# Kernel tuning notes

Hardware: AMD Instinct MI355X
Metric: run time of the kernel (lower is better)

Reference implementation:

```python
import jax, jax.numpy as jnp
import numpy as np

N, D_IN, H, C, K = 16384, 2048, 4096, 256, 256


def setup_inputs() -> dict:
    key = jax.random.key(0)
    ks = jax.random.split(key, 13)

    def lin(kw, kb, fan_in, fan_out):
        # torch Linear default init: U(-1/sqrt(fan_in), 1/sqrt(fan_in)); stored as [in, out]
        bound = 1.0 / np.sqrt(fan_in)
        W = jax.random.uniform(kw, (fan_in, fan_out), jnp.float32, -bound, bound)
        b = jax.random.uniform(kb, (fan_out,), jnp.float32, -bound, bound)
        return W, b

    W_e1, b_e1 = lin(ks[0], ks[1], D_IN, H)
    W_e2, b_e2 = lin(ks[2], ks[3], H, C)
    W_d1, b_d1 = lin(ks[4], ks[5], C, H)
    W_d2, b_d2 = lin(ks[6], ks[7], H, D_IN)
    # codebooks init U(-1/K, 1/K) per the torch code
    cb1 = jax.random.uniform(ks[8], (K, C), jnp.float32, -1.0 / K, 1.0 / K)
    cb2 = jax.random.uniform(ks[9], (K, C), jnp.float32, -1.0 / K, 1.0 / K)
    cb3 = jax.random.uniform(ks[10], (K, C), jnp.float32, -1.0 / K, 1.0 / K)
    x = jax.random.normal(ks[11], (N, D_IN), jnp.float32)
    return {"x": x, "W_e1": W_e1, "b_e1": b_e1, "W_e2": W_e2, "b_e2": b_e2,
            "cb1": cb1, "cb2": cb2, "cb3": cb3,
            "W_d1": W_d1, "b_d1": b_d1, "W_d2": W_d2, "b_d2": b_d2}


def _vq_stage(z, cb):
    # dist[n,k] = sum_c (cb[k,c] - z[n,c])^2 = ||z||^2 - 2 z.cb^T + ||cb||^2
    # (same math as the torch N x K x C broadcast, expressed as a GEMM)
    d = (jnp.sum(z * z, axis=1, keepdims=True)
         - 2.0 * (z @ cb.T)
         + jnp.sum(cb * cb, axis=1))            # [N, K]
    nearest = jnp.argmin(d, axis=1)             # [N]
    zq = cb[nearest]                            # gather [N, C]
    return nearest, zq


def reference(x, W_e1, b_e1, W_e2, b_e2, cb1, cb2, cb3, W_d1, b_d1, W_d2, b_d2):
    ze_1 = jax.nn.relu(x @ W_e1 + b_e1) @ W_e2 + b_e2     # [N, C]
    nearest_1, zq_1 = _vq_stage(ze_1, cb1)
    ze_2 = ze_1 - zq_1
    nearest_2, zq_2 = _vq_stage(ze_2, cb2)
    ze_3 = ze_2 - zq_2
    nearest_3, zq_3 = _vq_stage(ze_3, cb3)
    # straight-through estimator
    decoder_input = ze_1 + jax.lax.stop_gradient(zq_1 + zq_2 + zq_3 - ze_1)
    x_hat = jax.nn.sigmoid(decoder_input @ W_d1 + b_d1) @ W_d2 + b_d2
    return (x_hat, ze_1, ze_2, ze_3, zq_1, zq_2, zq_3, nearest_1, nearest_2, nearest_3)
```

## Files before the change

kernel.cpp:

```cpp
#include <hip/hip_runtime.h>
#include <cstddef>


#define NN 16384
#define DIN 2048
#define HH 4096
#define CC 256
#define QRED ((size_t)4096 * 256)
#define NZ 24

typedef unsigned short ushortT;
typedef __attribute__((ext_vector_type(8))) short bf16x8;
typedef __attribute__((ext_vector_type(4))) float f32x4;

__device__ __forceinline__ ushortT f2b(float v) {
    unsigned int u = __float_as_uint(v);
    return (ushortT)((u + 0x7fffu + ((u >> 16) & 1u)) >> 16);
}
__device__ __forceinline__ float b2f(ushortT s) {
    return __uint_as_float(((unsigned int)s) << 16);
}
__device__ __forceinline__ void split3(float v, ushortT& h, ushortT& m, ushortT& l) {
    h = f2b(v);
    float r1 = v - b2f(h);
    m = f2b(r1);
    l = f2b(r1 - b2f(m));
}

__device__ __forceinline__ void gld16(const void* g, void* l) {
    __builtin_amdgcn_global_load_lds(
        (const __attribute__((address_space(1))) unsigned int*)g,
        (__attribute__((address_space(3))) unsigned int*)l,
        16, 0, 0);
}

template<int NP>
__launch_bounds__(256)
__global__ void tsplit(const float* __restrict__ W,
                       ushortT* __restrict__ T0,
                       ushortT* __restrict__ T1,
                       ushortT* __restrict__ T2,
                       int K, int N)
{
    __shared__ float tile[32][33];
    const int k0 = blockIdx.y * 32, n0 = blockIdx.x * 32;
    const int c = threadIdx.x & 31, r = threadIdx.x >> 5;
    #pragma unroll
    for (int i = 0; i < 4; ++i)
        tile[r + 8*i][c] = W[(size_t)(k0 + r + 8*i) * N + n0 + c];
    __syncthreads();
    #pragma unroll
    for (int i = 0; i < 4; ++i) {
        const int nl = r + 8*i, kl = c;
        float v = tile[kl][nl];
        size_t o = (size_t)(n0 + nl) * K + k0 + kl;
        ushortT h = f2b(v);
        T0[o] = h;
        if (NP > 1) {
            float r1 = v - b2f(h);
            ushortT m = f2b(r1);
            T1[o] = m;
            T2[o] = f2b(r1 - b2f(m));
        }
    }
}

__launch_bounds__(256)
__global__ void split_src(const float* __restrict__ X,
                          ushortT* __restrict__ P0, ushortT* __restrict__ P1,
                          ushortT* __restrict__ P2, size_t n4)
{
    for (size_t i = (size_t)blockIdx.x * 256 + threadIdx.x; i < n4;
         i += (size_t)gridDim.x * 256) {
        float4 v = *(const float4*)(X + i * 4);
        ushort4 hv, mv, lv;
        split3(v.x, ((ushortT*)&hv)[0], ((ushortT*)&mv)[0], ((ushortT*)&lv)[0]);
        split3(v.y, ((ushortT*)&hv)[1], ((ushortT*)&mv)[1], ((ushortT*)&lv)[1]);
        split3(v.z, ((ushortT*)&hv)[2], ((ushortT*)&mv)[2], ((ushortT*)&lv)[2]);
        split3(v.w, ((ushortT*)&hv)[3], ((ushortT*)&mv)[3], ((ushortT*)&lv)[3]);
        *(ushort4*)(P0 + i * 4) = hv;
        *(ushort4*)(P1 + i * 4) = mv;
        *(ushort4*)(P2 + i * 4) = lv;
    }
}

template<int NSEG, int KSH, int NTC, int EPI, int OM>
__launch_bounds__(256, 2)
__global__ void gemm128(const ushortT* __restrict__ Ab, size_t aPl,
                        const ushortT* __restrict__ Bb, size_t bPl,
                        const float* __restrict__ bias,
                        float* __restrict__ Cf,
                        ushortT* __restrict__ Ob, size_t oPl,
                        int N, int K)
{
    __shared__ ushortT sh[24576];

    const int t    = threadIdx.x;
    const int lane = t & 63;
    const int wid  = t >> 6;
    const int l15  = lane & 15;
    const int l4   = lane >> 4;
    const int bm   = blockIdx.y * 128;
    const int bn   = blockIdx.x * 256;
    const int wn   = wid * 64;
    const int t0   = (OM == 3) ? blockIdx.z * NTC : 0;

    constexpr unsigned PA_PACK = 0x210100u;
    constexpr unsigned PB_PACK = 0x012010u;

    unsigned gA[2], gB[4];
    #pragma unroll
    for (int i = 0; i < 2; ++i) {
        const int c = i * 256 + t;
        const int row = c >> 2, slot = c & 3;
        const int colsw = (slot ^ ((row >> 1) & 3)) * 8;
        gA[i] = (unsigned)(bm + row) * (unsigned)K + colsw;
    }
    #pragma unroll
    for (int i = 0; i < 4; ++i) {
        const int c = i * 256 + t;
        const int row = c >> 2, slot = c & 3;
        const int colsw = (slot ^ ((row >> 1) & 3)) * 8;
        gB[i] = (unsigned)(bn + row) * (unsigned)K + colsw;
    }

    auto stage = [&](int buf, int gtt) {
        const int seg = (NSEG > 1) ? (gtt >> KSH) : 0;
        const unsigned kin = ((unsigned)(gtt & ((1 << KSH) - 1))) << 5;
        const unsigned pa = (NSEG > 1) ? ((PA_PACK >> (seg * 4)) & 15u) : 0u;
        const unsigned pb = (NSEG > 1) ? ((PB_PACK >> (seg * 4)) & 15u) : 0u;
        const ushortT* Abase = Ab + (size_t)pa * aPl + kin;
        const ushortT* Bbase = Bb + (size_t)pb * bPl + kin;
        ushortT* lb = sh + buf * 12288;
        #pragma unroll
        for (int i = 0; i < 2; ++i)
            gld16(Abase + gA[i], lb + (i * 256 + t) * 8);
        #pragma unroll
        for (int i = 0; i < 4; ++i)
            gld16(Bbase + gB[i], lb + 4096 + (i * 256 + t) * 8);
    };

    f32x4 acc[8][4] = {};

    stage(0, t0);

    #pragma unroll 1
    for (int tt = 0; tt < NTC; ++tt) {
        const int buf = tt & 1;
        const ushortT* As = sh + buf * 12288;
        const ushortT* Bs = As + 4096;
        const bool notlast = (tt + 1 < NTC);
        bf16x8 a_[8], b_[4];

        asm volatile("s_waitcnt vmcnt(0)" ::: "memory");
        __builtin_amdgcn_sched_barrier(0);
        __builtin_amdgcn_s_barrier();
        __builtin_amdgcn_sched_barrier(0);

        #pragma unroll
        for (int ni = 0; ni < 4; ++ni) {
            const int rb = wn + ni * 16 + l15;
            b_[ni] = *(const bf16x8*)&Bs[rb * 32 + (l4 ^ ((rb >> 1) & 3)) * 8];
        }
        #pragma unroll
        for (int mi = 0; mi < 8; ++mi) {
            const int ra = mi * 16 + l15;
            a_[mi] = *(const bf16x8*)&As[ra * 32 + (l4 ^ ((ra >> 1) & 3)) * 8];
        }
        if (notlast) stage(buf ^ 1, t0 + tt + 1);
        __builtin_amdgcn_sched_barrier(0);
        asm volatile("s_waitcnt lgkmcnt(0)" ::: "memory");
        __builtin_amdgcn_sched_barrier(0);
        __builtin_amdgcn_s_setprio(1);
        #pragma unroll
        for (int mi = 0; mi < 8; ++mi)
            #pragma unroll
            for (int ni = 0; ni < 4; ++ni)
                acc[mi][ni] = __builtin_amdgcn_mfma_f32_16x16x32_bf16(
                    a_[mi], b_[ni], acc[mi][ni], 0, 0, 0);
        __builtin_amdgcn_s_setprio(0);
        __builtin_amdgcn_sched_barrier(0);
    }

    #pragma unroll
    for (int ni = 0; ni < 4; ++ni) {
        const int gcol = bn + wn + ni * 16 + l15;
        float bvv = 0.0f;
        if (OM != 3) bvv = bias[gcol];
        #pragma unroll
        for (int mi = 0; mi < 8; ++mi) {
            #pragma unroll
            for (int r = 0; r < 4; ++r) {
                const int grow = bm + mi * 16 + l4 * 4 + r;
                const size_t o = (size_t)grow * N + gcol;
                if (OM == 3) {
                    Cf[(size_t)blockIdx.z * oPl + o] = acc[mi][ni][r];
                } else {
                    float v = acc[mi][ni][r] + bvv;
                    if (EPI == 1) v = fmaxf(v, 0.0f);
                    if (EPI == 2) v = 1.0f / (1.0f + expf(-v));
                    if (OM == 0) {
                        Cf[o] = v;
                    } else if (OM == 2) {
                        Ob[o] = f2b(v);
                    } else {
                        ushortT hh, mm, ll;
                        split3(v, hh, mm, ll);
                        Ob[o] = hh; Ob[oPl + o] = mm; Ob[2 * oPl + o] = ll;
                    }
                }
            }
        }
    }
}

__launch_bounds__(256)
__global__ void reduce_z(const float* __restrict__ part,
                         const float* __restrict__ bias,
                         float* __restrict__ outp, int n4)
{
    const int i = blockIdx.x * 256 + threadIdx.x;
    if (i >= n4) return;
    float4 s = *(const float4*)(part + (size_t)i * 4);
    #pragma unroll
    for (int z = 1; z < NZ; ++z) {
        float4 p = *(const float4*)(part + (size_t)z * (QRED) + (size_t)i * 4);
        s.x = __fadd_rn(s.x, p.x); s.y = __fadd_rn(s.y, p.y);
        s.z = __fadd_rn(s.z, p.z); s.w = __fadd_rn(s.w, p.w);
    }
    const int c4 = (i * 4) & 255;
    float4 b = *(const float4*)(bias + c4);
    s.x = __fadd_rn(s.x, b.x); s.y = __fadd_rn(s.y, b.y);
    s.z = __fadd_rn(s.z, b.z); s.w = __fadd_rn(s.w, b.w);
    *(float4*)(outp + (size_t)i * 4) = s;
}

__launch_bounds__(256)
__global__ void vq_kernel(const float* __restrict__ ze1,
                          const float* __restrict__ cb1,
                          const float* __restrict__ cb2,
                          const float* __restrict__ cb3,
                          float* __restrict__ out_ze2, float* __restrict__ out_ze3,
                          float* __restrict__ out_zq1, float* __restrict__ out_zq2,
                          float* __restrict__ out_zq3,
                          float* __restrict__ out_n1,  float* __restrict__ out_n2,
                          float* __restrict__ out_n3,
                          ushortT* __restrict__ dec_p)
{
    __shared__ float Zs[16][260];
    __shared__ float Ds[16][260];
    __shared__ float DecS[16][260];
    __shared__ float Srow[16];
    __shared__ int   Kmin[16];

    const int t    = threadIdx.x;
    const int row0 = blockIdx.x * 16;

    for (int i = t; i < 16*64; i += 256) {
        int r = i >> 6, c4 = (i & 63) << 2;
        float4 v = *(const float4*)(ze1 + (size_t)(row0 + r) * 256 + c4);
        *(float4*)&Zs[r][c4] = v;
        float4 z = {0.f,0.f,0.f,0.f};
        *(float4*)&DecS[r][c4] = z;
    }
    __syncthreads();

    const float* cbs[3] = {cb1, cb2, cb3};
    float* zqs[3] = {out_zq1, out_zq2, out_zq3};
    float* nss[3] = {out_n1, out_n2, out_n3};

    for (int s = 0; s < 3; ++s) {
        const float* cb = cbs[s];
        if (t < 16) {
            float ssum = 0.f;
            for (int c = 0; c < 256; ++c) ssum = fmaf(Zs[t][c], Zs[t][c], ssum);
            Srow[t] = ssum;
        }
        __syncthreads();
        {
            float accr[16];
            #pragma unroll
            for (int r = 0; r < 16; ++r) accr[r] = 0.f;
            float c2 = 0.f;
            const float* cbrow = cb + (size_t)t * 256;
            for (int c4 = 0; c4 < 256; c4 += 4) {
                float4 cv = *(const float4*)(cbrow + c4);
                c2 = fmaf(cv.x,cv.x,fmaf(cv.y,cv.y,fmaf(cv.z,cv.z,fmaf(cv.w,cv.w,c2))));
                #pragma unroll
                for (int r = 0; r < 16; ++r) {
                    float4 zv = *(const float4*)&Zs[r][c4];
                    accr[r] = fmaf(zv.x,cv.x,fmaf(zv.y,cv.y,
                              fmaf(zv.z,cv.z,fmaf(zv.w,cv.w,accr[r]))));
                }
            }
            #pragma unroll
            for (int r = 0; r < 16; ++r) {
                float g2 = __fmul_rn(2.0f, accr[r]);
                float t1 = __fsub_rn(Srow[r], g2);
                Ds[r][t]  = __fadd_rn(t1, c2);
            }
        }
        __syncthreads();
        if (t < 16) {
            float best = Ds[t][0];
            int bk = 0;
            for (int k = 1; k < 256; ++k) {
                float v = Ds[t][k];
                if (v < best) { best = v; bk = k; }
            }
            Kmin[t] = bk;
            nss[s][row0 + t] = (float)bk;
        }
        __syncthreads();
        for (int i = t; i < 16*64; i += 256) {
            int r = i >> 6, c4 = (i & 63) << 2;
            const float* q = cb + (size_t)Kmin[r] * 256 + c4;
            float4 qv = *(const float4*)q;
            *(float4*)&zqs[s][(size_t)(row0 + r) * 256 + c4] = qv;
            float4 dv = *(float4*)&DecS[r][c4];
            dv.x = __fadd_rn(dv.x, qv.x); dv.y = __fadd_rn(dv.y, qv.y);
            dv.z = __fadd_rn(dv.z, qv.z); dv.w = __fadd_rn(dv.w, qv.w);
            *(float4*)&DecS[r][c4] = dv;
            if (s < 2) {
                float4 zv = *(float4*)&Zs[r][c4];
                zv.x = __fsub_rn(zv.x, qv.x); zv.y = __fsub_rn(zv.y, qv.y);
                zv.z = __fsub_rn(zv.z, qv.z); zv.w = __fsub_rn(zv.w, qv.w);
                *(float4*)&Zs[r][c4] = zv;
                float* oz = (s == 0) ? out_ze2 : out_ze3;
                *(float4*)&oz[(size_t)(row0 + r) * 256 + c4] = zv;
            }
        }
        __syncthreads();
    }

    for (int i = t; i < 16*64; i += 256) {
        int r = i >> 6, c4 = (i & 63) << 2;
        float4 z1 = *(const float4*)(ze1 + (size_t)(row0 + r) * 256 + c4);
        float4 dv = *(float4*)&DecS[r][c4];
        float4 o;
        o.x = __fadd_rn(z1.x, __fsub_rn(dv.x, z1.x));
        o.y = __fadd_rn(z1.y, __fsub_rn(dv.y, z1.y));
        o.z = __fadd_rn(z1.z, __fsub_rn(dv.z, z1.z));
        o.w = __fadd_rn(z1.w, __fsub_rn(dv.w, z1.w));
        ushort4 ov;
        ((ushortT*)&ov)[0] = f2b(o.x);
        ((ushortT*)&ov)[1] = f2b(o.y);
        ((ushortT*)&ov)[2] = f2b(o.z);
        ((ushortT*)&ov)[3] = f2b(o.w);
        *(ushort4*)(dec_p + (size_t)(row0 + r) * 256 + c4) = ov;
    }
}

extern "C" void kernel_launch(void* const* d_in, const int* in_sizes, int n_in,
                              void* d_out, int out_size, void* d_ws, size_t ws_size,
                              hipStream_t stream)
{
    const float* x   = (const float*)d_in[0];
    const float* We1 = (const float*)d_in[1];
    const float* be1 = (const float*)d_in[2];
    const float* We2 = (const float*)d_in[3];
    const float* be2 = (const float*)d_in[4];
    const float* cb1 = (const float*)d_in[5];
    const float* cb2 = (const float*)d_in[6];
    const float* cb3 = (const float*)d_in[7];
    const float* Wd1 = (const float*)d_in[8];
    const float* bd1 = (const float*)d_in[9];
    const float* Wd2 = (const float*)d_in[10];
    const float* bd2 = (const float*)d_in[11];

    float* out   = (float*)d_out;
    float* x_hat = out;
    float* ze1   = out + 33554432;
    float* ze2   = out + 37748736;
    float* ze3   = out + 41943040;
    float* zq1   = out + 46137344;
    float* zq2   = out + 50331648;
    float* zq3   = out + 54525952;
    float* n1    = out + 58720256;
    float* n2    = out + 58736640;
    float* n3    = out + 58753024;

    const int    QR   = 4096;
    const size_t szXq = (size_t)QR * DIN;
    const size_t szHq = (size_t)QR * HH;
    const size_t szW1 = (size_t)HH * DIN;
    const size_t szW2 = (size_t)CC * HH;

    ushortT* xq   = (ushortT*)d_ws;
    ushortT* hq   = xq + 3 * szXq;
    ushortT* We1t = hq + 3 * szHq;
    ushortT* We2t = We1t + 3 * szW1;
    ushortT* Wd1t = We2t + 3 * szW2;
    ushortT* Wd2t = Wd1t + szW2;
    ushortT* decp = Wd2t + szW1;
    float*   zpart = (float*)(decp + (size_t)NN * CC);
    ushortT* h2p  = xq;

    dim3 blk(256);

    tsplit<3><<<dim3(HH/32, DIN/32), blk, 0, stream>>>(We1, We1t, We1t+szW1, We1t+2*szW1, DIN, HH);
    tsplit<3><<<dim3(CC/32, HH/32),  blk, 0, stream>>>(We2, We2t, We2t+szW2, We2t+2*szW2, HH, CC);
    tsplit<1><<<dim3(HH/32, CC/32),  blk, 0, stream>>>(Wd1, Wd1t, nullptr, nullptr, CC, HH);
    tsplit<1><<<dim3(DIN/32, HH/32), blk, 0, stream>>>(Wd2, Wd2t, nullptr, nullptr, HH, DIN);

    for (int q = 0; q < 4; ++q) {
        split_src<<<dim3(2048), blk, 0, stream>>>(x + (size_t)q * szXq,
                                                  xq, xq + szXq, xq + 2*szXq, szXq / 4);
        gemm128<6,6,384,1,1><<<dim3(HH/256, QR/128), blk, 0, stream>>>(
            xq, szXq, We1t, szW1, be1, nullptr, hq, szHq, HH, DIN);
        gemm128<6,7,32,0,3><<<dim3(CC/256, QR/128, NZ), blk, 0, stream>>>(
            hq, szHq, We2t, szW2, nullptr, zpart, nullptr, QRED, CC, HH);
        reduce_z<<<dim3(QR*CC/4/256), blk, 0, stream>>>(
            zpart, be2, ze1 + (size_t)q * QR * CC, QR*CC/4);
    }

    vq_kernel<<<dim3(NN/16), blk, 0, stream>>>(ze1, cb1, cb2, cb3,
                                               ze2, ze3, zq1, zq2, zq3,
                                               n1, n2, n3, decp);

    gemm128<1,3,8,2,2><<<dim3(HH/256, NN/128), blk, 0, stream>>>(
        decp, 0, Wd1t, 0, bd1, nullptr, h2p, 0, HH, CC);
    gemm128<1,7,128,0,0><<<dim3(DIN/256, NN/128), blk, 0, stream>>>(
        h2p, 0, Wd2t, 0, bd2, x_hat, nullptr, 0, DIN, HH);
}
```

Baseline: 2.692 ms.

## Load B operand directly to registers and double K-tile depth per stage

The GEMM kernel now stages only the A tile through LDS, with a 64-wide K step and an 8-way XOR swizzle. Each wave loads its own B fragments straight from global memory into registers, double-buffered across an unrolled pair of iterations. The vmcnt wait is relaxed so the B prefetch can stay in flight. The aim is to cut LDS traffic and size and halve barrier count per K. The cost is more register pressure and uncoalesced-ish direct B loads that can add global latency.

```diff
diff --git a/kernel.cpp b/kernel.cpp
--- a/kernel.cpp
+++ b/kernel.cpp
@@ -86,14 +86,14 @@
 
 template<int NSEG, int KSH, int NTC, int EPI, int OM>
 __launch_bounds__(256, 2)
-__global__ void gemm128(const ushortT* __restrict__ Ab, size_t aPl,
-                        const ushortT* __restrict__ Bb, size_t bPl,
-                        const float* __restrict__ bias,
-                        float* __restrict__ Cf,
-                        ushortT* __restrict__ Ob, size_t oPl,
-                        int N, int K)
-{
-    __shared__ ushortT sh[24576];
+__global__ void gemmD(const ushortT* __restrict__ Ab, size_t aPl,
+                      const ushortT* __restrict__ Bb, size_t bPl,
+                      const float* __restrict__ bias,
+                      float* __restrict__ Cf,
+                      ushortT* __restrict__ Ob, size_t oPl,
+                      int N, int K)
+{
+    __shared__ ushortT sh[16384];
 
     const int t    = threadIdx.x;
     const int lane = t & 63;
@@ -108,78 +108,92 @@
     constexpr unsigned PA_PACK = 0x210100u;
     constexpr unsigned PB_PACK = 0x012010u;
 
-    unsigned gA[2], gB[4];
-    #pragma unroll
-    for (int i = 0; i < 2; ++i) {
-        const int c = i * 256 + t;
-        const int row = c >> 2, slot = c & 3;
-        const int colsw = (slot ^ ((row >> 1) & 3)) * 8;
-        gA[i] = (unsigned)(bm + row) * (unsigned)K + colsw;
-    }
+    unsigned gA[4];
     #pragma unroll
     for (int i = 0; i < 4; ++i) {
         const int c = i * 256 + t;
-        const int row = c >> 2, slot = c & 3;
-        const int colsw = (slot ^ ((row >> 1) & 3)) * 8;
-        gB[i] = (unsigned)(bn + row) * (unsigned)K + colsw;
-    }
-
-    auto stage = [&](int buf, int gtt) {
+        const int row = c >> 3, slot = c & 7;
+        gA[i] = (unsigned)(bm + row) * (unsigned)K + (slot ^ (row & 7)) * 8;
+    }
+    unsigned gBrow[4];
+    #pragma unroll
+    for (int ni = 0; ni < 4; ++ni)
+        gBrow[ni] = (unsigned)(bn + wn + ni * 16 + l15) * (unsigned)K + l4 * 8;
+
+    auto stageA = [&](int buf, int gtt) {
         const int seg = (NSEG > 1) ? (gtt >> KSH) : 0;
-        const unsigned kin = ((unsigned)(gtt & ((1 << KSH) - 1))) << 5;
+        const unsigned kin = ((unsigned)(gtt & ((1 << KSH) - 1))) << 6;
         const unsigned pa = (NSEG > 1) ? ((PA_PACK >> (seg * 4)) & 15u) : 0u;
-        const unsigned pb = (NSEG > 1) ? ((PB_PACK >> (seg * 4)) & 15u) : 0u;
         const ushortT* Abase = Ab + (size_t)pa * aPl + kin;
-        const ushortT* Bbase = Bb + (size_t)pb * bPl + kin;
-        ushortT* lb = sh + buf * 12288;
-        #pragma unroll
-        for (int i = 0; i < 2; ++i)
-            gld16(Abase + gA[i], lb + (i * 256 + t) * 8);
+        ushortT* lb = sh + buf * 8192;
         #pragma unroll
         for (int i = 0; i < 4; ++i)
-            gld16(Bbase + gB[i], lb + 4096 + (i * 256 + t) * 8);
+            gld16(Abase + gA[i], lb + (i * 256 + t) * 8);
     };
+    auto loadB = [&](bf16x8 (&br)[8], int gtt) {
+        const int seg = (NSEG > 1) ? (gtt >> KSH) : 0;
+        const unsigned kin = ((unsigned)(gtt & ((1 << KSH) - 1))) << 6;
+        const unsigned pb = (NSEG > 1) ? ((PB_PACK >> (seg * 4)) & 15u) : 0u;
+        const ushortT* Bbase = Bb + (size_t)pb * bPl + kin;
+        #pragma unroll
+        for (int kk = 0; kk < 2; ++kk)
+            #pragma unroll
+            for (int ni = 0; ni < 4; ++ni)
+                br[kk * 4 + ni] = *(const bf16x8*)(Bbase + gBrow[ni] + kk * 32);
+    };
 
     f32x4 acc[8][4] = {};
-
-    stage(0, t0);
+    bf16x8 bA[8], bB[8];
+
+    stageA(0, t0);
+    loadB(bA, t0);
 
     #pragma unroll 1
-    for (int tt = 0; tt < NTC; ++tt) {
-        const int buf = tt & 1;
-        const ushortT* As = sh + buf * 12288;
-        const ushortT* Bs = As + 4096;
-        const bool notlast = (tt + 1 < NTC);
-        bf16x8 a_[8], b_[4];
-
-        asm volatile("s_waitcnt vmcnt(0)" ::: "memory");
-        __builtin_amdgcn_sched_barrier(0);
-        __builtin_amdgcn_s_barrier();
-        __builtin_amdgcn_sched_barrier(0);
-
+    for (int tt2 = 0; tt2 < NTC; tt2 += 2) {
         #pragma unroll
-        for (int ni = 0; ni < 4; ++ni) {
-            const int rb = wn + ni * 16 + l15;
-            b_[ni] = *(const bf16x8*)&Bs[rb * 32 + (l4 ^ ((rb >> 1) & 3)) * 8];
-        }
-        #pragma unroll
-        for (int mi = 0; mi < 8; ++mi) {
-            const int ra = mi * 16 + l15;
-            a_[mi] = *(const bf16x8*)&As[ra * 32 + (l4 ^ ((ra >> 1) & 3)) * 8];
-        }
-        if (notlast) stage(buf ^ 1, t0 + tt + 1);
-        __builtin_amdgcn_sched_barrier(0);
-        asm volatile("s_waitcnt lgkmcnt(0)" ::: "memory");
-        __builtin_amdgcn_sched_barrier(0);
-        __builtin_amdgcn_s_setprio(1);
-        #pragma unroll
-        for (int mi = 0; mi < 8; ++mi)
-            #pragma unroll
-            for (int ni = 0; ni < 4; ++ni)
-                acc[mi][ni] = __builtin_amdgcn_mfma_f32_16x16x32_bf16(
-                    a_[mi], b_[ni], acc[mi][ni], 0, 0, 0);
-        __builtin_amdgcn_s_setprio(0);
-        __builtin_amdgcn_sched_barrier(0);
+        for (int sub = 0; sub < 2; ++sub) {
+            const int tt  = tt2 + sub;
+            const int buf = sub;
+            const ushortT* As = sh + buf * 8192;
+            const bool notlast = (tt + 1 < NTC);
+            bf16x8 a_[16];
+
+            if (notlast) { asm volatile("s_waitcnt vmcnt(8)" ::: "memory"); }
+            else         { asm volatile("s_waitcnt vmcnt(0)" ::: "memory"); }
+            __builtin_amdgcn_sched_barrier(0);
+            __builtin_amdgcn_s_barrier();
+            __builtin_amdgcn_sched_barrier(0);
+
+            #pragma unroll
+            for (int kk = 0; kk < 2; ++kk)
+                #pragma unroll
+                for (int mi = 0; mi < 8; ++mi) {
+                    const int ra = mi * 16 + l15;
+                    a_[kk * 8 + mi] = *(const bf16x8*)
+                        &As[ra * 64 + ((((kk << 2) | l4)) ^ (ra & 7)) * 8];
+                }
+            if (notlast) {
+                stageA(buf ^ 1, t0 + tt + 1);
+                if (sub == 0) loadB(bB, t0 + tt + 1);
+                else          loadB(bA, t0 + tt + 1);
+            }
+            __builtin_amdgcn_sched_barrier(0);
+            asm volatile("s_waitcnt lgkmcnt(0)" ::: "memory");
+            __builtin_amdgcn_sched_barrier(0);
+            __builtin_amdgcn_s_setprio(1);
+            #pragma unroll
+            for (int kk = 0; kk < 2; ++kk)
+                #pragma unroll
+                for (int mi = 0; mi < 8; ++mi)
+                    #pragma unroll
+                    for (int ni = 0; ni < 4; ++ni)
+                        acc[mi][ni] = __builtin_amdgcn_mfma_f32_16x16x32_bf16(
+                            a_[kk * 8 + mi],
+                            (sub == 0) ? bA[kk * 4 + ni] : bB[kk * 4 + ni],
+                            acc[mi][ni], 0, 0, 0);
+            __builtin_amdgcn_s_setprio(0);
+            __builtin_amdgcn_sched_barrier(0);
+        }
     }
 
     #pragma unroll
@@ -406,9 +420,9 @@
     for (int q = 0; q < 4; ++q) {
         split_src<<<dim3(2048), blk, 0, stream>>>(x + (size_t)q * szXq,
                                                   xq, xq + szXq, xq + 2*szXq, szXq / 4);
-        gemm128<6,6,384,1,1><<<dim3(HH/256, QR/128), blk, 0, stream>>>(
+        gemmD<6,5,192,1,1><<<dim3(HH/256, QR/128), blk, 0, stream>>>(
             xq, szXq, We1t, szW1, be1, nullptr, hq, szHq, HH, DIN);
-        gemm128<6,7,32,0,3><<<dim3(CC/256, QR/128, NZ), blk, 0, stream>>>(
+        gemmD<6,6,16,0,3><<<dim3(CC/256, QR/128, NZ), blk, 0, stream>>>(
             hq, szHq, We2t, szW2, nullptr, zpart, nullptr, QRED, CC, HH);
         reduce_z<<<dim3(QR*CC/4/256), blk, 0, stream>>>(
             zpart, be2, ze1 + (size_t)q * QR * CC, QR*CC/4);
@@ -418,8 +432,8 @@
                                                ze2, ze3, zq1, zq2, zq3,
                                                n1, n2, n3, decp);
 
-    gemm128<1,3,8,2,2><<<dim3(HH/256, NN/128), blk, 0, stream>>>(
+    gemmD<1,2,4,2,2><<<dim3(HH/256, NN/128), blk, 0, stream>>>(
         decp, 0, Wd1t, 0, bd1, nullptr, h2p, 0, HH, CC);
-    gemm128<1,7,128,0,0><<<dim3(DIN/256, NN/128), blk, 0, stream>>>(
+    gemmD<1,6,64,0,0><<<dim3(DIN/256, NN/128), blk, 0, stream>>>(
         h2p, 0, Wd2t, 0, bd2, x_hat, nullptr, 0, DIN, HH);
 }
```

After: 8.399 ms. 212% more time.

## Split GEMM tile across eight waves with 2x4 warp layout

Applied to the files above, without the earlier changes.

The 128x256 GEMM tile goes from 4 waves (each 128x64) to 8 waves in a 2x4 grid (each 64x64), halving per-wave accumulators and A-fragment registers. Global-to-LDS loads are redistributed over 512 threads. A fragments are now loaded per mi inside the MFMA loop instead of all up front, and the explicit lgkmcnt wait and setprio are dropped. The aim is more waves per CU and more latency hiding, at the cost of each wave reloading B fragments and less MFMA work per LDS read.

```diff
diff --git a/kernel.cpp b/kernel.cpp
--- a/kernel.cpp
+++ b/kernel.cpp
@@ -85,13 +85,13 @@
 }
 
 template<int NSEG, int KSH, int NTC, int EPI, int OM>
-__launch_bounds__(256, 2)
-__global__ void gemm128(const ushortT* __restrict__ Ab, size_t aPl,
-                        const ushortT* __restrict__ Bb, size_t bPl,
-                        const float* __restrict__ bias,
-                        float* __restrict__ Cf,
-                        ushortT* __restrict__ Ob, size_t oPl,
-                        int N, int K)
+__launch_bounds__(512, 4)
+__global__ void gemmW(const ushortT* __restrict__ Ab, size_t aPl,
+                      const ushortT* __restrict__ Bb, size_t bPl,
+                      const float* __restrict__ bias,
+                      float* __restrict__ Cf,
+                      ushortT* __restrict__ Ob, size_t oPl,
+                      int N, int K)
 {
     __shared__ ushortT sh[24576];
 
@@ -102,26 +102,23 @@
     const int l4   = lane >> 4;
     const int bm   = blockIdx.y * 128;
     const int bn   = blockIdx.x * 256;
-    const int wn   = wid * 64;
+    const int wm   = (wid >> 2) * 64;
+    const int wn   = (wid & 3) * 64;
     const int t0   = (OM == 3) ? blockIdx.z * NTC : 0;
 
     constexpr unsigned PA_PACK = 0x210100u;
     constexpr unsigned PB_PACK = 0x012010u;
 
-    unsigned gA[2], gB[4];
+    unsigned gA, gB[2];
+    {
+        const int row = t >> 2, slot = t & 3;
+        gA = (unsigned)(bm + row) * (unsigned)K + (slot ^ ((row >> 1) & 3)) * 8;
+    }
     #pragma unroll
     for (int i = 0; i < 2; ++i) {
-        const int c = i * 256 + t;
+        const int c = i * 512 + t;
         const int row = c >> 2, slot = c & 3;
-        const int colsw = (slot ^ ((row >> 1) & 3)) * 8;
-        gA[i] = (unsigned)(bm + row) * (unsigned)K + colsw;
-    }
-    #pragma unroll
-    for (int i = 0; i < 4; ++i) {
-        const int c = i * 256 + t;
-        const int row = c >> 2, slot = c & 3;
-        const int colsw = (slot ^ ((row >> 1) & 3)) * 8;
-        gB[i] = (unsigned)(bn + row) * (unsigned)K + colsw;
+        gB[i] = (unsigned)(bn + row) * (unsigned)K + (slot ^ ((row >> 1) & 3)) * 8;
     }
 
     auto stage = [&](int buf, int gtt) {
@@ -132,15 +129,13 @@
         const ushortT* Abase = Ab + (size_t)pa * aPl + kin;
         const ushortT* Bbase = Bb + (size_t)pb * bPl + kin;
         ushortT* lb = sh + buf * 12288;
+        gld16(Abase + gA, lb + t * 8);
         #pragma unroll
         for (int i = 0; i < 2; ++i)
-            gld16(Abase + gA[i], lb + (i * 256 + t) * 8);
-        #pragma unroll
-        for (int i = 0; i < 4; ++i)
-            gld16(Bbase + gB[i], lb + 4096 + (i * 256 + t) * 8);
+            gld16(Bbase + gB[i], lb + 4096 + (i * 512 + t) * 8);
     };
 
-    f32x4 acc[8][4] = {};
+    f32x4 acc[4][4] = {};
 
     stage(0, t0);
 
@@ -150,35 +145,28 @@
         const ushortT* As = sh + buf * 12288;
         const ushortT* Bs = As + 4096;
         const bool notlast = (tt + 1 < NTC);
-        bf16x8 a_[8], b_[4];
 
         asm volatile("s_waitcnt vmcnt(0)" ::: "memory");
         __builtin_amdgcn_sched_barrier(0);
         __builtin_amdgcn_s_barrier();
         __builtin_amdgcn_sched_barrier(0);
 
+        bf16x8 b_[4];
         #pragma unroll
         for (int ni = 0; ni < 4; ++ni) {
             const int rb = wn + ni * 16 + l15;
             b_[ni] = *(const bf16x8*)&Bs[rb * 32 + (l4 ^ ((rb >> 1) & 3)) * 8];
         }
+        if (notlast) stage(buf ^ 1, t0 + tt + 1);
         #pragma unroll
-        for (int mi = 0; mi < 8; ++mi) {
-            const int ra = mi * 16 + l15;
-            a_[mi] = *(const bf16x8*)&As[ra * 32 + (l4 ^ ((ra >> 1) & 3)) * 8];
-        }
-        if (notlast) stage(buf ^ 1, t0 + tt + 1);
-        __builtin_amdgcn_sched_barrier(0);
-        asm volatile("s_waitcnt lgkmcnt(0)" ::: "memory");
-        __builtin_amdgcn_sched_barrier(0);
-        __builtin_amdgcn_s_setprio(1);
-        #pragma unroll
-        for (int mi = 0; mi < 8; ++mi)
+        for (int mi = 0; mi < 4; ++mi) {
+            const int ra = wm + mi * 16 + l15;
+            bf16x8 a_ = *(const bf16x8*)&As[ra * 32 + (l4 ^ ((ra >> 1) & 3)) * 8];
             #pragma unroll
             for (int ni = 0; ni < 4; ++ni)
                 acc[mi][ni] = __builtin_amdgcn_mfma_f32_16x16x32_bf16(
-                    a_[mi], b_[ni], acc[mi][ni], 0, 0, 0);
-        __builtin_amdgcn_s_setprio(0);
+                    a_, b_[ni], acc[mi][ni], 0, 0, 0);
+        }
         __builtin_amdgcn_sched_barrier(0);
     }
 
@@ -188,10 +176,10 @@
         float bvv = 0.0f;
         if (OM != 3) bvv = bias[gcol];
         #pragma unroll
-        for (int mi = 0; mi < 8; ++mi) {
+        for (int mi = 0; mi < 4; ++mi) {
             #pragma unroll
             for (int r = 0; r < 4; ++r) {
-                const int grow = bm + mi * 16 + l4 * 4 + r;
+                const int grow = bm + wm + mi * 16 + l4 * 4 + r;
                 const size_t o = (size_t)grow * N + gcol;
                 if (OM == 3) {
                     Cf[(size_t)blockIdx.z * oPl + o] = acc[mi][ni][r];
@@ -396,7 +384,7 @@
     float*   zpart = (float*)(decp + (size_t)NN * CC);
     ushortT* h2p  = xq;
 
-    dim3 blk(256);
+    dim3 blk(256), blk5(512);
 
     tsplit<3><<<dim3(HH/32, DIN/32), blk, 0, stream>>>(We1, We1t, We1t+szW1, We1t+2*szW1, DIN, HH);
     tsplit<3><<<dim3(CC/32, HH/32),  blk, 0, stream>>>(We2, We2t, We2t+szW2, We2t+2*szW2, HH, CC);
@@ -406,9 +394,9 @@
     for (int q = 0; q < 4; ++q) {
         split_src<<<dim3(2048), blk, 0, stream>>>(x + (size_t)q * szXq,
                                                   xq, xq + szXq, xq + 2*szXq, szXq / 4);
-        gemm128<6,6,384,1,1><<<dim3(HH/256, QR/128), blk, 0, stream>>>(
+        gemmW<6,6,384,1,1><<<dim3(HH/256, QR/128), blk5, 0, stream>>>(
             xq, szXq, We1t, szW1, be1, nullptr, hq, szHq, HH, DIN);
-        gemm128<6,7,32,0,3><<<dim3(CC/256, QR/128, NZ), blk, 0, stream>>>(
+        gemmW<6,7,32,0,3><<<dim3(CC/256, QR/128, NZ), blk5, 0, stream>>>(
             hq, szHq, We2t, szW2, nullptr, zpart, nullptr, QRED, CC, HH);
         reduce_z<<<dim3(QR*CC/4/256), blk, 0, stream>>>(
             zpart, be2, ze1 + (size_t)q * QR * CC, QR*CC/4);
@@ -418,8 +406,8 @@
                                                ze2, ze3, zq1, zq2, zq3,
                                                n1, n2, n3, decp);
 
-    gemm128<1,3,8,2,2><<<dim3(HH/256, NN/128), blk, 0, stream>>>(
+    gemmW<1,3,8,2,2><<<dim3(HH/256, NN/128), blk5, 0, stream>>>(
         decp, 0, Wd1t, 0, bd1, nullptr, h2p, 0, HH, CC);
-    gemm128<1,7,128,0,0><<<dim3(DIN/256, NN/128), blk, 0, stream>>>(
+    gemmW<1,7,128,0,0><<<dim3(DIN/256, NN/128), blk5, 0, stream>>>(
         h2p, 0, Wd2t, 0, bd2, x_hat, nullptr, 0, DIN, HH);
 }
```

Result: no change. 2.715 ms (+0.9%).

## Enlarge GEMM tile to 256x256 with 512 threads and triple-buffered LDS pipeline

Applied to the files above, without the earlier changes.

The bf16 MFMA GEMM moves from 128x256 tiles with 4 waves to 256x256 tiles with 8 waves arranged 2x4, halving the number of blocks and the global traffic per output element. The LDS staging becomes a three-buffer ring that prefetches two k-steps ahead, with a single vmcnt-gated barrier per iteration instead of the previous wait-all and barrier. The split-K count for the encoder's second GEMM drops from 24 to 16, with more k-tiles per slice. The 96KB of shared memory per block likely limits occupancy to one block per CU, which trades latency hiding for reuse.

```diff
diff --git a/kernel.cpp b/kernel.cpp
--- a/kernel.cpp
+++ b/kernel.cpp
@@ -7,7 +7,7 @@
 #define HH 4096
 #define CC 256
 #define QRED ((size_t)4096 * 256)
-#define NZ 24
+#define NZ 16
 
 typedef unsigned short ushortT;
 typedef __attribute__((ext_vector_type(8))) short bf16x8;
@@ -85,42 +85,37 @@
 }
 
 template<int NSEG, int KSH, int NTC, int EPI, int OM>
-__launch_bounds__(256, 2)
-__global__ void gemm128(const ushortT* __restrict__ Ab, size_t aPl,
-                        const ushortT* __restrict__ Bb, size_t bPl,
-                        const float* __restrict__ bias,
-                        float* __restrict__ Cf,
-                        ushortT* __restrict__ Ob, size_t oPl,
-                        int N, int K)
-{
-    __shared__ ushortT sh[24576];
+__launch_bounds__(512, 2)
+__global__ void gemmT(const ushortT* __restrict__ Ab, size_t aPl,
+                      const ushortT* __restrict__ Bb, size_t bPl,
+                      const float* __restrict__ bias,
+                      float* __restrict__ Cf,
+                      ushortT* __restrict__ Ob, size_t oPl,
+                      int N, int K)
+{
+    __shared__ ushortT sh[49152];
 
     const int t    = threadIdx.x;
     const int lane = t & 63;
     const int wid  = t >> 6;
     const int l15  = lane & 15;
     const int l4   = lane >> 4;
-    const int bm   = blockIdx.y * 128;
+    const int bm   = blockIdx.y * 256;
     const int bn   = blockIdx.x * 256;
-    const int wn   = wid * 64;
+    const int wm   = (wid >> 2) * 128;
+    const int wn   = (wid & 3) * 64;
     const int t0   = (OM == 3) ? blockIdx.z * NTC : 0;
 
     constexpr unsigned PA_PACK = 0x210100u;
     constexpr unsigned PB_PACK = 0x012010u;
 
-    unsigned gA[2], gB[4];
+    unsigned gA[2], gB[2];
     #pragma unroll
     for (int i = 0; i < 2; ++i) {
-        const int c = i * 256 + t;
+        const int c = i * 512 + t;
         const int row = c >> 2, slot = c & 3;
         const int colsw = (slot ^ ((row >> 1) & 3)) * 8;
         gA[i] = (unsigned)(bm + row) * (unsigned)K + colsw;
-    }
-    #pragma unroll
-    for (int i = 0; i < 4; ++i) {
-        const int c = i * 256 + t;
-        const int row = c >> 2, slot = c & 3;
-        const int colsw = (slot ^ ((row >> 1) & 3)) * 8;
         gB[i] = (unsigned)(bn + row) * (unsigned)K + colsw;
     }
 
@@ -131,32 +126,29 @@
         const unsigned pb = (NSEG > 1) ? ((PB_PACK >> (seg * 4)) & 15u) : 0u;
         const ushortT* Abase = Ab + (size_t)pa * aPl + kin;
         const ushortT* Bbase = Bb + (size_t)pb * bPl + kin;
-        ushortT* lb = sh + buf * 12288;
+        ushortT* lb = sh + (size_t)buf * 16384;
         #pragma unroll
         for (int i = 0; i < 2; ++i)
-            gld16(Abase + gA[i], lb + (i * 256 + t) * 8);
-        #pragma unroll
-        for (int i = 0; i < 4; ++i)
-            gld16(Bbase + gB[i], lb + 4096 + (i * 256 + t) * 8);
+            gld16(Abase + gA[i], lb + (i * 512 + t) * 8);
+        #pragma unroll
+        for (int i = 0; i < 2; ++i)
+            gld16(Bbase + gB[i], lb + 8192 + (i * 512 + t) * 8);
     };
 
     f32x4 acc[8][4] = {};
 
     stage(0, t0);
+    stage(1, t0 + 1);
+    asm volatile("s_waitcnt vmcnt(4)" ::: "memory");
+    __builtin_amdgcn_s_barrier();
 
     #pragma unroll 1
     for (int tt = 0; tt < NTC; ++tt) {
-        const int buf = tt & 1;
-        const ushortT* As = sh + buf * 12288;
-        const ushortT* Bs = As + 4096;
-        const bool notlast = (tt + 1 < NTC);
-        bf16x8 a_[8], b_[4];
-
-        asm volatile("s_waitcnt vmcnt(0)" ::: "memory");
-        __builtin_amdgcn_sched_barrier(0);
-        __builtin_amdgcn_s_barrier();
-        __builtin_amdgcn_sched_barrier(0);
-
+        const ushortT* As = sh + (size_t)(tt % 3) * 16384;
+        const ushortT* Bs = As + 8192;
+        const bool deep = (tt + 2 < NTC);
+
+        bf16x8 b_[4], a_[8];
         #pragma unroll
         for (int ni = 0; ni < 4; ++ni) {
             const int rb = wn + ni * 16 + l15;
@@ -164,13 +156,11 @@
         }
         #pragma unroll
         for (int mi = 0; mi < 8; ++mi) {
-            const int ra = mi * 16 + l15;
+            const int ra = wm + mi * 16 + l15;
             a_[mi] = *(const bf16x8*)&As[ra * 32 + (l4 ^ ((ra >> 1) & 3)) * 8];
         }
-        if (notlast) stage(buf ^ 1, t0 + tt + 1);
-        __builtin_amdgcn_sched_barrier(0);
-        asm volatile("s_waitcnt lgkmcnt(0)" ::: "memory");
-        __builtin_amdgcn_sched_barrier(0);
+        if (deep) stage((tt + 2) % 3, t0 + tt + 2);
+
         __builtin_amdgcn_s_setprio(1);
         #pragma unroll
         for (int mi = 0; mi < 8; ++mi)
@@ -179,7 +169,10 @@
                 acc[mi][ni] = __builtin_amdgcn_mfma_f32_16x16x32_bf16(
                     a_[mi], b_[ni], acc[mi][ni], 0, 0, 0);
         __builtin_amdgcn_s_setprio(0);
-        __builtin_amdgcn_sched_barrier(0);
+
+        if (deep) { asm volatile("s_waitcnt vmcnt(4)" ::: "memory"); }
+        else      { asm volatile("s_waitcnt vmcnt(0)" ::: "memory"); }
+        __builtin_amdgcn_s_barrier();
     }
 
     #pragma unroll
@@ -191,7 +184,7 @@
         for (int mi = 0; mi < 8; ++mi) {
             #pragma unroll
             for (int r = 0; r < 4; ++r) {
-                const int grow = bm + mi * 16 + l4 * 4 + r;
+                const int grow = bm + wm + mi * 16 + l4 * 4 + r;
                 const size_t o = (size_t)grow * N + gcol;
                 if (OM == 3) {
                     Cf[(size_t)blockIdx.z * oPl + o] = acc[mi][ni][r];
@@ -396,7 +389,7 @@
     float*   zpart = (float*)(decp + (size_t)NN * CC);
     ushortT* h2p  = xq;
 
-    dim3 blk(256);
+    dim3 blk(256), blk5(512);
 
     tsplit<3><<<dim3(HH/32, DIN/32), blk, 0, stream>>>(We1, We1t, We1t+szW1, We1t+2*szW1, DIN, HH);
     tsplit<3><<<dim3(CC/32, HH/32),  blk, 0, stream>>>(We2, We2t, We2t+szW2, We2t+2*szW2, HH, CC);
@@ -406,9 +399,9 @@
     for (int q = 0; q < 4; ++q) {
         split_src<<<dim3(2048), blk, 0, stream>>>(x + (size_t)q * szXq,
                                                   xq, xq + szXq, xq + 2*szXq, szXq / 4);
-        gemm128<6,6,384,1,1><<<dim3(HH/256, QR/128), blk, 0, stream>>>(
+        gemmT<6,6,384,1,1><<<dim3(HH/256, QR/256), blk5, 0, stream>>>(
             xq, szXq, We1t, szW1, be1, nullptr, hq, szHq, HH, DIN);
-        gemm128<6,7,32,0,3><<<dim3(CC/256, QR/128, NZ), blk, 0, stream>>>(
+        gemmT<6,7,48,0,3><<<dim3(CC/256, QR/256, NZ), blk5, 0, stream>>>(
             hq, szHq, We2t, szW2, nullptr, zpart, nullptr, QRED, CC, HH);
         reduce_z<<<dim3(QR*CC/4/256), blk, 0, stream>>>(
             zpart, be2, ze1 + (size_t)q * QR * CC, QR*CC/4);
@@ -418,8 +411,8 @@
                                                ze2, ze3, zq1, zq2, zq3,
                                                n1, n2, n3, decp);
 
-    gemm128<1,3,8,2,2><<<dim3(HH/256, NN/128), blk, 0, stream>>>(
+    gemmT<1,3,8,2,2><<<dim3(HH/256, NN/256), blk5, 0, stream>>>(
         decp, 0, Wd1t, 0, bd1, nullptr, h2p, 0, HH, CC);
-    gemm128<1,7,128,0,0><<<dim3(DIN/256, NN/128), blk, 0, stream>>>(
+    gemmT<1,7,128,0,0><<<dim3(DIN/256, NN/256), blk5, 0, stream>>>(
         h2p, 0, Wd2t, 0, bd2, x_hat, nullptr, 0, DIN, HH);
 }
```

After: 2.492 ms. 7.4% less time.
